# Kernel optimization log

Hardware: AMD Instinct MI355X
Metric: run time of the kernel (lower is better)

Reference implementation:

```python
import jax, jax.numpy as jnp
import numpy as np

H = 1024
V = 128000


def setup_inputs() -> dict:
    key = jax.random.key(0)
    ks = jax.random.split(key, 9)
    s = 0.02  # param init scale for numerical sanity
    return {
        "input_ids": jax.random.randint(ks[0], (1,), 0, V),
        "hidden": jax.random.normal(ks[1], (1, 1, H), dtype=jnp.float32),
        "emb": jax.random.normal(ks[2], (V, H), dtype=jnp.float32) * s,
        "W_ih": jax.random.normal(ks[3], (3 * H, H), dtype=jnp.float32) * s,
        "W_hh": jax.random.normal(ks[4], (3 * H, H), dtype=jnp.float32) * s,
        "b_ih": jax.random.normal(ks[5], (3 * H,), dtype=jnp.float32) * s,
        "b_hh": jax.random.normal(ks[6], (3 * H,), dtype=jnp.float32) * s,
        "W_out": jax.random.normal(ks[7], (V, H), dtype=jnp.float32) * s,
        "b_out": jax.random.normal(ks[8], (V,), dtype=jnp.float32) * s,
    }


def reference(input_ids, hidden, emb, W_ih, W_hh, b_ih, b_hh, W_out, b_out):
    # embedding lookup for the single token, then ReLU (matches F.relu on embed)
    x = jax.nn.relu(emb[input_ids[0]])            # (H,)
    h0 = hidden[0, 0]                             # (H,)
    # PyTorch GRU cell: gates ordered [r, z, n]
    gi = W_ih @ x + b_ih                          # (3H,)
    gh = W_hh @ h0 + b_hh                         # (3H,)
    r = jax.nn.sigmoid(gi[:H] + gh[:H])
    z = jax.nn.sigmoid(gi[H:2 * H] + gh[H:2 * H])
    n = jnp.tanh(gi[2 * H:] + r * gh[2 * H:])
    h1 = (1.0 - z) * n + z * h0                   # (H,)
    # output projection + log-softmax over vocab (dim=1 on (1, V))
    logits = W_out @ h1 + b_out                   # (V,)
    logp = jax.nn.log_softmax(logits)[None, :]    # (1, V)
    return logp, h1[None, None, :]                # ((1,V), (1,1,H))
```

## Files before the change

### kernel.cpp

```cpp
#include <hip/hip_runtime.h>
#include <math.h>

#define H 1024
#define V 128000
#define G3H 3072

#define WS_GI   0
#define WS_GH   G3H
#define WS_GMAX (2*G3H)
#define WS_LSE  (2*G3H + 1)

__global__ __launch_bounds__(256) void gates_matvec(
    const int* __restrict__ ids, const float* __restrict__ hidden,
    const float* __restrict__ emb,
    const float* __restrict__ W_ih, const float* __restrict__ W_hh,
    const float* __restrict__ b_ih, const float* __restrict__ b_hh,
    float* __restrict__ ws) {
  const int wid  = (blockIdx.x * blockDim.x + threadIdx.x) >> 6;
  const int lane = threadIdx.x & 63;
  const int id   = ids[0];

  const bool isGi = (wid < G3H);
  const int  row  = isGi ? wid : (wid - G3H);

  const float4* w = (const float4*)((isGi ? W_ih : W_hh) + (size_t)row * H);
  const float4* v = (const float4*)(isGi ? (emb + (size_t)id * H) : hidden);

  float sum = 0.f;
#pragma unroll
  for (int k = 0; k < 4; ++k) {
    float4 wv = w[lane + 64 * k];
    float4 xv = v[lane + 64 * k];
    if (isGi) {
      xv.x = fmaxf(xv.x, 0.f); xv.y = fmaxf(xv.y, 0.f);
      xv.z = fmaxf(xv.z, 0.f); xv.w = fmaxf(xv.w, 0.f);
    }
    sum = fmaf(wv.x, xv.x, sum);
    sum = fmaf(wv.y, xv.y, sum);
    sum = fmaf(wv.z, xv.z, sum);
    sum = fmaf(wv.w, xv.w, sum);
  }
#pragma unroll
  for (int off = 32; off > 0; off >>= 1) sum += __shfl_down(sum, off);

  if (lane == 0) {
    const float b = isGi ? b_ih[row] : b_hh[row];
    ws[wid] = sum + b;
  }
}

__global__ __launch_bounds__(256) void gru_gate(
    const float* __restrict__ hidden, const float* __restrict__ ws,
    float* __restrict__ d_out) {
  const int i = blockIdx.x * blockDim.x + threadIdx.x;
  const float* gi = ws + WS_GI;
  const float* gh = ws + WS_GH;
  const float r = 1.f / (1.f + expf(-(gi[i]           + gh[i])));
  const float z = 1.f / (1.f + expf(-(gi[H + i]       + gh[H + i])));
  const float n = tanhf(gi[2 * H + i] + r * gh[2 * H + i]);
  const float h0 = hidden[i];
  d_out[V + i] = (1.f - z) * n + z * h0;
}

__global__ __launch_bounds__(256) void logits_matvec(
    const float* __restrict__ W_out, const float* __restrict__ b_out,
    float* __restrict__ d_out) {
  __shared__ float4 h1s[256];
  h1s[threadIdx.x] = ((const float4*)(d_out + V))[threadIdx.x];
  __syncthreads();

  const int lane = threadIdx.x & 63;
  const int row  = blockIdx.x * 4 + (threadIdx.x >> 6);
  const float4* w = (const float4*)(W_out + (size_t)row * H);

  float sum = 0.f;
#pragma unroll
  for (int k = 0; k < 4; ++k) {
    const float4 wv = w[lane + 64 * k];
    const float4 xv = h1s[lane + 64 * k];
    sum = fmaf(wv.x, xv.x, sum);
    sum = fmaf(wv.y, xv.y, sum);
    sum = fmaf(wv.z, xv.z, sum);
    sum = fmaf(wv.w, xv.w, sum);
  }
#pragma unroll
  for (int off = 32; off > 0; off >>= 1) sum += __shfl_down(sum, off);

  if (lane == 0) d_out[row] = sum + b_out[row];
}

__global__ __launch_bounds__(1024) void lse_reduce(
    const float* __restrict__ logits, float* __restrict__ ws) {
  __shared__ float red[1024];
  const int t = threadIdx.x;
  const float4* l4 = (const float4*)logits;

  float m = -INFINITY;
  for (int i = t; i < V / 4; i += 1024) {
    const float4 v = l4[i];
    m = fmaxf(m, fmaxf(fmaxf(v.x, v.y), fmaxf(v.z, v.w)));
  }
  red[t] = m;
  __syncthreads();
  for (int s = 512; s > 0; s >>= 1) {
    if (t < s) red[t] = fmaxf(red[t], red[t + s]);
    __syncthreads();
  }
  const float gmax = red[0];
  __syncthreads();

  float sum = 0.f;
  for (int i = t; i < V / 4; i += 1024) {
    const float4 v = l4[i];
    sum += expf(v.x - gmax) + expf(v.y - gmax) + expf(v.z - gmax) + expf(v.w - gmax);
  }
  red[t] = sum;
  __syncthreads();
  for (int s = 512; s > 0; s >>= 1) {
    if (t < s) red[t] += red[t + s];
    __syncthreads();
  }
  if (t == 0) {
    ws[WS_GMAX] = gmax;
    ws[WS_LSE]  = logf(red[0]);
  }
}

__global__ __launch_bounds__(256) void logp_write(
    float* __restrict__ d_out, const float* __restrict__ ws) {
  const int v = blockIdx.x * blockDim.x + threadIdx.x;
  const float gmax = ws[WS_GMAX];
  const float lse  = ws[WS_LSE];
  d_out[v] = d_out[v] - gmax - lse;
}

extern "C" void kernel_launch(void* const* d_in, const int* in_sizes, int n_in,
                              void* d_out, int out_size, void* d_ws, size_t ws_size,
                              hipStream_t stream) {
  const int*   ids    = (const int*)d_in[0];
  const float* hidden = (const float*)d_in[1];
  const float* emb    = (const float*)d_in[2];
  const float* W_ih   = (const float*)d_in[3];
  const float* W_hh   = (const float*)d_in[4];
  const float* b_ih   = (const float*)d_in[5];
  const float* b_hh   = (const float*)d_in[6];
  const float* W_out  = (const float*)d_in[7];
  const float* b_out  = (const float*)d_in[8];
  float* out = (float*)d_out;
  float* ws  = (float*)d_ws;

  gates_matvec<<<1536, 256, 0, stream>>>(ids, hidden, emb, W_ih, W_hh, b_ih, b_hh, ws);
  gru_gate<<<4, 256, 0, stream>>>(hidden, ws, out);
  logits_matvec<<<V / 4, 256, 0, stream>>>(W_out, b_out, out);
  lse_reduce<<<1, 1024, 0, stream>>>(out, ws);
  logp_write<<<V / 256, 256, 0, stream>>>(out, ws);
}
```

Before: 121.1 us.

## Fuse GRU gate into logits matvec with online LSE partials

```diff
diff --git a/kernel.cpp b/kernel.cpp
--- a/kernel.cpp
+++ b/kernel.cpp
@@ -4,11 +4,11 @@
 #define H 1024
 #define V 128000
 #define G3H 3072
+#define NW2A 4000
 
 #define WS_GI   0
 #define WS_GH   G3H
-#define WS_GMAX (2*G3H)
-#define WS_LSE  (2*G3H + 1)
+#define WS_PART 8192
 
 __global__ __launch_bounds__(256) void gates_matvec(
     const int* __restrict__ ids, const float* __restrict__ hidden,
@@ -16,122 +16,130 @@
     const float* __restrict__ W_ih, const float* __restrict__ W_hh,
     const float* __restrict__ b_ih, const float* __restrict__ b_hh,
     float* __restrict__ ws) {
-  const int wid  = (blockIdx.x * blockDim.x + threadIdx.x) >> 6;
-  const int lane = threadIdx.x & 63;
-  const int id   = ids[0];
+  const int tid  = threadIdx.x;
+  const int lane = tid & 63;
+  const int wid  = blockIdx.x * 4 + (tid >> 6);
+  const bool isGi = (wid < 512);
+  const int row0 = (isGi ? wid : wid - 512) * 6;
 
-  const bool isGi = (wid < G3H);
-  const int  row  = isGi ? wid : (wid - G3H);
+  const float* Wm = isGi ? W_ih : W_hh;
+  const float* xp = isGi ? (emb + (size_t)ids[0] * H) : hidden;
 
-  const float4* w = (const float4*)((isGi ? W_ih : W_hh) + (size_t)row * H);
-  const float4* v = (const float4*)(isGi ? (emb + (size_t)id * H) : hidden);
+  float4 x0 = ((const float4*)xp)[lane];
+  float4 x1 = ((const float4*)xp)[lane + 64];
+  float4 x2 = ((const float4*)xp)[lane + 128];
+  float4 x3 = ((const float4*)xp)[lane + 192];
+  if (isGi) {
+    x0.x=fmaxf(x0.x,0.f); x0.y=fmaxf(x0.y,0.f); x0.z=fmaxf(x0.z,0.f); x0.w=fmaxf(x0.w,0.f);
+    x1.x=fmaxf(x1.x,0.f); x1.y=fmaxf(x1.y,0.f); x1.z=fmaxf(x1.z,0.f); x1.w=fmaxf(x1.w,0.f);
+    x2.x=fmaxf(x2.x,0.f); x2.y=fmaxf(x2.y,0.f); x2.z=fmaxf(x2.z,0.f); x2.w=fmaxf(x2.w,0.f);
+    x3.x=fmaxf(x3.x,0.f); x3.y=fmaxf(x3.y,0.f); x3.z=fmaxf(x3.z,0.f); x3.w=fmaxf(x3.w,0.f);
+  }
 
-  float sum = 0.f;
+#pragma unroll 2
+  for (int r = 0; r < 6; ++r) {
+    const int row = row0 + r;
+    const float4* w = (const float4*)(Wm + (size_t)row * H);
+    const float4 a = w[lane];
+    const float4 b = w[lane + 64];
+    const float4 c = w[lane + 128];
+    const float4 d = w[lane + 192];
+    float p0 = fmaf(a.x,x0.x, fmaf(a.y,x0.y, fmaf(a.z,x0.z, a.w*x0.w)));
+    float p1 = fmaf(b.x,x1.x, fmaf(b.y,x1.y, fmaf(b.z,x1.z, b.w*x1.w)));
+    float p2 = fmaf(c.x,x2.x, fmaf(c.y,x2.y, fmaf(c.z,x2.z, c.w*x2.w)));
+    float p3 = fmaf(d.x,x3.x, fmaf(d.y,x3.y, fmaf(d.z,x3.z, d.w*x3.w)));
+    float s = (p0 + p1) + (p2 + p3);
 #pragma unroll
-  for (int k = 0; k < 4; ++k) {
-    float4 wv = w[lane + 64 * k];
-    float4 xv = v[lane + 64 * k];
-    if (isGi) {
-      xv.x = fmaxf(xv.x, 0.f); xv.y = fmaxf(xv.y, 0.f);
-      xv.z = fmaxf(xv.z, 0.f); xv.w = fmaxf(xv.w, 0.f);
+    for (int off = 1; off < 64; off <<= 1) s += __shfl_xor(s, off);
+    if (lane == 0) {
+      if (isGi) ws[WS_GI + row] = s + b_ih[row];
+      else      ws[WS_GH + row] = s + b_hh[row];
     }
-    sum = fmaf(wv.x, xv.x, sum);
-    sum = fmaf(wv.y, xv.y, sum);
-    sum = fmaf(wv.z, xv.z, sum);
-    sum = fmaf(wv.w, xv.w, sum);
-  }
-#pragma unroll
-  for (int off = 32; off > 0; off >>= 1) sum += __shfl_down(sum, off);
-
-  if (lane == 0) {
-    const float b = isGi ? b_ih[row] : b_hh[row];
-    ws[wid] = sum + b;
   }
 }
 
-__global__ __launch_bounds__(256) void gru_gate(
-    const float* __restrict__ hidden, const float* __restrict__ ws,
-    float* __restrict__ d_out) {
-  const int i = blockIdx.x * blockDim.x + threadIdx.x;
-  const float* gi = ws + WS_GI;
-  const float* gh = ws + WS_GH;
-  const float r = 1.f / (1.f + expf(-(gi[i]           + gh[i])));
-  const float z = 1.f / (1.f + expf(-(gi[H + i]       + gh[H + i])));
-  const float n = tanhf(gi[2 * H + i] + r * gh[2 * H + i]);
-  const float h0 = hidden[i];
-  d_out[V + i] = (1.f - z) * n + z * h0;
-}
+__global__ __launch_bounds__(256) void logits_lse(
+    const float* __restrict__ hidden, const float* __restrict__ ws_in,
+    const float* __restrict__ W_out, const float* __restrict__ b_out,
+    float* __restrict__ d_out, float* __restrict__ ws_part) {
+  __shared__ float h1s[H];
+  const int tid = threadIdx.x;
 
-__global__ __launch_bounds__(256) void logits_matvec(
-    const float* __restrict__ W_out, const float* __restrict__ b_out,
-    float* __restrict__ d_out) {
-  __shared__ float4 h1s[256];
-  h1s[threadIdx.x] = ((const float4*)(d_out + V))[threadIdx.x];
+  for (int i = tid; i < H; i += 256) {
+    const float r = 1.f / (1.f + expf(-(ws_in[WS_GI + i]       + ws_in[WS_GH + i])));
+    const float z = 1.f / (1.f + expf(-(ws_in[WS_GI + H + i]   + ws_in[WS_GH + H + i])));
+    const float n = tanhf(ws_in[WS_GI + 2*H + i] + r * ws_in[WS_GH + 2*H + i]);
+    h1s[i] = (1.f - z) * n + z * hidden[i];
+  }
   __syncthreads();
+  if (blockIdx.x == 0) {
+    for (int i = tid; i < H; i += 256) d_out[V + i] = h1s[i];
+  }
 
-  const int lane = threadIdx.x & 63;
-  const int row  = blockIdx.x * 4 + (threadIdx.x >> 6);
-  const float4* w = (const float4*)(W_out + (size_t)row * H);
+  const int lane = tid & 63;
+  const int wid  = blockIdx.x * 4 + (tid >> 6);
+  const int row0 = wid * 32;
 
-  float sum = 0.f;
+  const float4 x0 = ((const float4*)h1s)[lane];
+  const float4 x1 = ((const float4*)h1s)[lane + 64];
+  const float4 x2 = ((const float4*)h1s)[lane + 128];
+  const float4 x3 = ((const float4*)h1s)[lane + 192];
+
+  float m = -INFINITY, S = 0.f;
+#pragma unroll 2
+  for (int r = 0; r < 32; ++r) {
+    const int row = row0 + r;
+    const float4* w = (const float4*)(W_out + (size_t)row * H);
+    const float4 a = w[lane];
+    const float4 b = w[lane + 64];
+    const float4 c = w[lane + 128];
+    const float4 d = w[lane + 192];
+    float p0 = fmaf(a.x,x0.x, fmaf(a.y,x0.y, fmaf(a.z,x0.z, a.w*x0.w)));
+    float p1 = fmaf(b.x,x1.x, fmaf(b.y,x1.y, fmaf(b.z,x1.z, b.w*x1.w)));
+    float p2 = fmaf(c.x,x2.x, fmaf(c.y,x2.y, fmaf(c.z,x2.z, c.w*x2.w)));
+    float p3 = fmaf(d.x,x3.x, fmaf(d.y,x3.y, fmaf(d.z,x3.z, d.w*x3.w)));
+    float s = (p0 + p1) + (p2 + p3);
 #pragma unroll
-  for (int k = 0; k < 4; ++k) {
-    const float4 wv = w[lane + 64 * k];
-    const float4 xv = h1s[lane + 64 * k];
-    sum = fmaf(wv.x, xv.x, sum);
-    sum = fmaf(wv.y, xv.y, sum);
-    sum = fmaf(wv.z, xv.z, sum);
-    sum = fmaf(wv.w, xv.w, sum);
+    for (int off = 1; off < 64; off <<= 1) s += __shfl_xor(s, off);
+    const float logit = s + b_out[row];
+    if (lane == 0) d_out[row] = logit;
+    const float mn = fmaxf(m, logit);
+    S = S * expf(m - mn) + expf(logit - mn);
+    m = mn;
   }
-#pragma unroll
-  for (int off = 32; off > 0; off >>= 1) sum += __shfl_down(sum, off);
-
-  if (lane == 0) d_out[row] = sum + b_out[row];
-}
-
-__global__ __launch_bounds__(1024) void lse_reduce(
-    const float* __restrict__ logits, float* __restrict__ ws) {
-  __shared__ float red[1024];
-  const int t = threadIdx.x;
-  const float4* l4 = (const float4*)logits;
-
-  float m = -INFINITY;
-  for (int i = t; i < V / 4; i += 1024) {
-    const float4 v = l4[i];
-    m = fmaxf(m, fmaxf(fmaxf(v.x, v.y), fmaxf(v.z, v.w)));
-  }
-  red[t] = m;
-  __syncthreads();
-  for (int s = 512; s > 0; s >>= 1) {
-    if (t < s) red[t] = fmaxf(red[t], red[t + s]);
-    __syncthreads();
-  }
-  const float gmax = red[0];
-  __syncthreads();
-
-  float sum = 0.f;
-  for (int i = t; i < V / 4; i += 1024) {
-    const float4 v = l4[i];
-    sum += expf(v.x - gmax) + expf(v.y - gmax) + expf(v.z - gmax) + expf(v.w - gmax);
-  }
-  red[t] = sum;
-  __syncthreads();
-  for (int s = 512; s > 0; s >>= 1) {
-    if (t < s) red[t] += red[t + s];
-    __syncthreads();
-  }
-  if (t == 0) {
-    ws[WS_GMAX] = gmax;
-    ws[WS_LSE]  = logf(red[0]);
+  if (lane == 0) {
+    ws_part[2 * wid]     = m;
+    ws_part[2 * wid + 1] = S;
   }
 }
 
-__global__ __launch_bounds__(256) void logp_write(
-    float* __restrict__ d_out, const float* __restrict__ ws) {
-  const int v = blockIdx.x * blockDim.x + threadIdx.x;
-  const float gmax = ws[WS_GMAX];
-  const float lse  = ws[WS_LSE];
-  d_out[v] = d_out[v] - gmax - lse;
+__global__ __launch_bounds__(256) void lse_norm(
+    float* __restrict__ d_out, const float* __restrict__ ws_part) {
+  __shared__ float redm[256], reds[256];
+  const int tid = threadIdx.x;
+
+  float m = -INFINITY, S = 0.f;
+  for (int b = tid; b < NW2A; b += 256) {
+    const float mb = ws_part[2*b], sb = ws_part[2*b+1];
+    const float mn = fmaxf(m, mb);
+    S = S * expf(m - mn) + sb * expf(mb - mn);
+    m = mn;
+  }
+  redm[tid] = m; reds[tid] = S;
+  __syncthreads();
+  for (int s = 128; s > 0; s >>= 1) {
+    if (tid < s) {
+      const float m2 = redm[tid + s], s2 = reds[tid + s];
+      const float mn = fmaxf(redm[tid], m2);
+      reds[tid] = reds[tid] * expf(redm[tid] - mn) + s2 * expf(m2 - mn);
+      redm[tid] = mn;
+    }
+    __syncthreads();
+  }
+  const float lse = redm[0] + logf(reds[0]);
+
+  const int i = blockIdx.x * 256 + tid;
+  d_out[i] -= lse;
 }
 
 extern "C" void kernel_launch(void* const* d_in, const int* in_sizes, int n_in,
@@ -149,9 +157,7 @@
   float* out = (float*)d_out;
   float* ws  = (float*)d_ws;
 
-  gates_matvec<<<1536, 256, 0, stream>>>(ids, hidden, emb, W_ih, W_hh, b_ih, b_hh, ws);
-  gru_gate<<<4, 256, 0, stream>>>(hidden, ws, out);
-  logits_matvec<<<V / 4, 256, 0, stream>>>(W_out, b_out, out);
-  lse_reduce<<<1, 1024, 0, stream>>>(out, ws);
-  logp_write<<<V / 256, 256, 0, stream>>>(out, ws);
+  gates_matvec<<<256, 256, 0, stream>>>(ids, hidden, emb, W_ih, W_hh, b_ih, b_hh, ws);
+  logits_lse<<<1000, 256, 0, stream>>>(hidden, ws, W_out, b_out, out, ws + WS_PART);
+  lse_norm<<<500, 256, 0, stream>>>(out, ws + WS_PART);
 }
```

New measurement: 134.1 us. +10.8%, slower.
